# Kernel tuning notes

Measured on AMD Instinct MI355X. Metric: run time of the kernel, lower is better.

The kernel has to match this reference:

```python
import jax, jax.numpy as jnp
import numpy as np

B, N, IN_DIM, HID = 32, 1024, 128, 64


def setup_inputs() -> dict:
    key = jax.random.key(0)
    ks = jax.random.split(key, 12)
    s_in = 1.0 / np.sqrt(IN_DIM)
    s_h = 1.0 / np.sqrt(HID)
    return {
        "x": jax.random.normal(ks[0], (B, N, IN_DIM), dtype=jnp.float32),
        "A": jax.random.uniform(ks[1], (B, N, N), dtype=jnp.float32),
        # fc_hidden: input_dim -> hidden_dim
        "W_h": jax.random.uniform(ks[2], (IN_DIM, HID), jnp.float32, -s_in, s_in),
        "b_h": jax.random.uniform(ks[3], (HID,), jnp.float32, -s_in, s_in),
        # fc_1 inside Gated_Skip_Connection (input_dim != output_dim)
        "W_fc1": jax.random.uniform(ks[4], (IN_DIM, HID), jnp.float32, -s_in, s_in),
        "b_fc1": jax.random.uniform(ks[5], (HID,), jnp.float32, -s_in, s_in),
        # gated_X1, gated_X2: hidden -> hidden
        "W_g1": jax.random.uniform(ks[6], (HID, HID), jnp.float32, -s_h, s_h),
        "b_g1": jax.random.uniform(ks[7], (HID,), jnp.float32, -s_h, s_h),
        "W_g2": jax.random.uniform(ks[8], (HID, HID), jnp.float32, -s_h, s_h),
        "b_g2": jax.random.uniform(ks[9], (HID,), jnp.float32, -s_h, s_h),
    }


def reference(x, A, W_h, b_h, W_fc1, b_fc1, W_g1, b_g1, W_g2, b_g2):
    # x_new = bmm(A, fc_hidden(x))   [B, N, HID]
    x_new = jnp.einsum("bnm,bmh->bnh", A, x @ W_h + b_h)
    # gated skip connection (input_dim != output_dim -> project x first)
    x_proj = x @ W_fc1 + b_fc1
    gate = jax.nn.sigmoid((x_proj @ W_g1 + b_g1) + (x_new @ W_g2 + b_g2))
    out = x_new * gate + x_proj * (1.0 - gate)
    return out
```

## Files before the change

### kernel.cpp

```cpp
#include <hip/hip_runtime.h>
#include <hip/hip_bf16.h>

#define NB 32
#define NN 1024
#define IND 128
#define HD 64

typedef float f32x4 __attribute__((ext_vector_type(4)));
typedef short bf16x8 __attribute__((ext_vector_type(8)));
typedef unsigned short ushortx4 __attribute__((ext_vector_type(4)));

union FragU { unsigned short us[8]; unsigned int u32[4]; bf16x8 v; };

__device__ __forceinline__ unsigned short f2bf(float f) {
    union { float f; unsigned u; } x; x.f = f;
    unsigned r = x.u + 0x7FFFu + ((x.u >> 16) & 1u);
    return (unsigned short)(r >> 16);
}
__device__ __forceinline__ float bf2f(unsigned short h) {
    union { unsigned u; float f; } x; x.u = ((unsigned)h) << 16; return x.f;
}
__device__ __forceinline__ unsigned int cvtpk(float lo, float hi) {
    unsigned int r;
    asm("v_cvt_pk_bf16_f32 %0, %1, %2" : "=v"(r) : "v"(lo), "v"(hi));
    return r;
}

__device__ __forceinline__ void gl16(void* lds, const void* g) {
    __builtin_amdgcn_global_load_lds(
        (const __attribute__((address_space(1))) unsigned int*)g,
        (__attribute__((address_space(3))) unsigned int*)lds, 16, 0, 0);
}

__global__ void prep_k(const float* __restrict__ W_h, const float* __restrict__ W_fc1,
                       const float* __restrict__ W_g1, const float* __restrict__ W_g2,
                       const float* __restrict__ b_g1, const float* __restrict__ b_g2,
                       unsigned short* __restrict__ WcT_hi, unsigned short* __restrict__ WcT_lo,
                       unsigned short* __restrict__ Wg1T_hi, unsigned short* __restrict__ Wg1T_lo,
                       unsigned short* __restrict__ Wg2T_hi, unsigned short* __restrict__ Wg2T_lo,
                       float* __restrict__ biasP1) {
    int t = blockIdx.x * blockDim.x + threadIdx.x;
    if (t < 16384) {
        int o = t >> 7, k = t & 127;
        float v = (o < 64) ? W_h[k * 64 + o] : W_fc1[k * 64 + (o - 64)];
        unsigned short hi = f2bf(v);
        WcT_hi[t] = hi; WcT_lo[t] = f2bf(v - bf2f(hi));
    } else if (t < 20480) {
        int r = t - 16384; int o = r >> 6, k = r & 63;
        float v = W_g1[k * 64 + o];
        unsigned short hi = f2bf(v);
        Wg1T_hi[r] = hi; Wg1T_lo[r] = f2bf(v - bf2f(hi));
    } else if (t < 24576) {
        int r = t - 20480; int o = r >> 6, k = r & 63;
        float v = W_g2[k * 64 + o];
        unsigned short hi = f2bf(v);
        Wg2T_hi[r] = hi; Wg2T_lo[r] = f2bf(v - bf2f(hi));
    } else if (t < 24640) {
        int j = t - 24576;
        biasP1[j] = b_g1[j] + b_g2[j];
    }
}

__global__ __launch_bounds__(64) void k1(
        const float* __restrict__ x,
        const unsigned short* __restrict__ WcT_hi, const unsigned short* __restrict__ WcT_lo,
        const unsigned short* __restrict__ Wg1T_hi, const unsigned short* __restrict__ Wg1T_lo,
        const float* __restrict__ b_h, const float* __restrict__ b_fc1,
        const float* __restrict__ biasP1,
        unsigned short* __restrict__ hF, float* __restrict__ xproj,
        float* __restrict__ p1) {
    __shared__ unsigned short lds_hi[16 * 64];
    __shared__ unsigned short lds_lo[16 * 64];

    const int lane = threadIdx.x;
    const int lr = lane & 15, lg = lane >> 4;
    const int blk = blockIdx.x;
    const int b = blk >> 6;
    const int n0 = (blk & 63) * 16;

    const float* xp = x + (size_t)(b * NN + n0 + lr) * IND;

    f32x4 xa[4][2];
#pragma unroll
    for (int ks = 0; ks < 4; ks++) {
        const f32x4* ap = (const f32x4*)(xp + 32 * ks + 8 * lg);
        xa[ks][0] = ap[0]; xa[ks][1] = ap[1];
    }

    f32x4 acc[8];
#pragma unroll
    for (int f = 0; f < 8; f++) acc[f] = (f32x4){0.f, 0.f, 0.f, 0.f};

#pragma unroll
    for (int ks = 0; ks < 4; ks++) {
        FragU ah, al;
#pragma unroll
        for (int i = 0; i < 4; i++) {
            unsigned short h0 = f2bf(xa[ks][0][i]); ah.us[i] = h0;     al.us[i]     = f2bf(xa[ks][0][i] - bf2f(h0));
            unsigned short h1 = f2bf(xa[ks][1][i]); ah.us[4 + i] = h1; al.us[4 + i] = f2bf(xa[ks][1][i] - bf2f(h1));
        }
#pragma unroll
        for (int f = 0; f < 8; f++) {
            int off = (16 * f + lr) * 128 + 32 * ks + 8 * lg;
            bf16x8 wh = *(const bf16x8*)(WcT_hi + off);
            bf16x8 wl = *(const bf16x8*)(WcT_lo + off);
            acc[f] = __builtin_amdgcn_mfma_f32_16x16x32_bf16(ah.v, wh, acc[f], 0, 0, 0);
            acc[f] = __builtin_amdgcn_mfma_f32_16x16x32_bf16(ah.v, wl, acc[f], 0, 0, 0);
            acc[f] = __builtin_amdgcn_mfma_f32_16x16x32_bf16(al.v, wh, acc[f], 0, 0, 0);
        }
    }

    const int mb = n0 + 4 * lg;
    const int tile = mb >> 5;
    const int lanepart = lr + 16 * ((mb >> 3) & 3);
    const int j0 = mb & 7;

#pragma unroll
    for (int f = 0; f < 4; f++) {
        int c = 16 * f + lr;
        float bh = b_h[c];
        ushortx4 hv;
#pragma unroll
        for (int r = 0; r < 4; r++) hv[r] = f2bf(acc[f][r] + bh);
        *(ushortx4*)(hF + (size_t)b * 65536 + (size_t)(tile * 4 + f) * 512 + lanepart * 8 + j0) = hv;
    }

#pragma unroll
    for (int f = 4; f < 8; f++) {
        int c = 16 * (f - 4) + lr;
        float bp = b_fc1[c];
#pragma unroll
        for (int r = 0; r < 4; r++) {
            float v = acc[f][r] + bp;
            int n = mb + r;
            xproj[(size_t)(b * NN + n) * 64 + c] = v;
            int ln = 4 * lg + r;
            int idx = ln * 64 + (((c >> 3) ^ (ln & 7)) << 3) + (c & 7);
            unsigned short hi = f2bf(v);
            lds_hi[idx] = hi;
            lds_lo[idx] = f2bf(v - bf2f(hi));
        }
    }
    __syncthreads();

    f32x4 accP[4];
#pragma unroll
    for (int f = 0; f < 4; f++) accP[f] = (f32x4){0.f, 0.f, 0.f, 0.f};
#pragma unroll
    for (int ks = 0; ks < 2; ks++) {
        int c0 = 32 * ks + 8 * lg;
        int idx = lr * 64 + (((c0 >> 3) ^ (lr & 7)) << 3);
        bf16x8 a_hi = *(const bf16x8*)(lds_hi + idx);
        bf16x8 a_lo = *(const bf16x8*)(lds_lo + idx);
#pragma unroll
        for (int f = 0; f < 4; f++) {
            int off = (16 * f + lr) * 64 + c0;
            bf16x8 b_hi = *(const bf16x8*)(Wg1T_hi + off);
            bf16x8 b_lo = *(const bf16x8*)(Wg1T_lo + off);
            accP[f] = __builtin_amdgcn_mfma_f32_16x16x32_bf16(a_hi, b_hi, accP[f], 0, 0, 0);
            accP[f] = __builtin_amdgcn_mfma_f32_16x16x32_bf16(a_hi, b_lo, accP[f], 0, 0, 0);
            accP[f] = __builtin_amdgcn_mfma_f32_16x16x32_bf16(a_lo, b_hi, accP[f], 0, 0, 0);
        }
    }
#pragma unroll
    for (int f = 0; f < 4; f++) {
        int c = 16 * f + lr;
        float bb = biasP1[c];
#pragma unroll
        for (int r = 0; r < 4; r++) {
            int n = mb + r;
            p1[(size_t)(b * NN + n) * 64 + c] = accP[f][r] + bb;
        }
    }
}

__global__ __launch_bounds__(256, 4) void k2(
        const float* __restrict__ A, const unsigned short* __restrict__ hF,
        const unsigned short* __restrict__ Wg2T_hi, const unsigned short* __restrict__ Wg2T_lo,
        const float* __restrict__ p1, const float* __restrict__ xproj,
        float* __restrict__ out) {
    __shared__ char smem[36864];

    const int tid = threadIdx.x;
    const int w = tid >> 6, lane = tid & 63;
    const int lr = lane & 15, lg = lane >> 4;

    const int bid = blockIdx.x;
    const int wgid = (bid & 7) * 128 + (bid >> 3);
    const int b = wgid >> 5;
    const int blkst = wgid & 31;

    const float* aS[4];
#pragma unroll
    for (int i = 0; i < 4; i++) {
        int rl = w * 4 + i;
        aS[i] = A + (size_t)(b * NN + blkst * 32 + rl) * NN + ((lane ^ rl) << 2);
    }
    const unsigned short* hp = hF + (size_t)b * 65536 + w * 512 + lane * 8;

    bf16x8 hb[8];

#pragma unroll
    for (int i = 0; i < 4; i++)
        gl16(smem + (w * 4 + i) * 1024, aS[i]);
#pragma unroll
    for (int ks = 0; ks < 8; ks++)
        hb[ks] = *(const bf16x8*)(hp + (size_t)ks * 2048);
    __syncthreads();

#define COMPUTE(ks, Abase)                                                     \
    {                                                                          \
        int g0 = (ks) * 8 + lg * 2;                                            \
        f32x4 a0 = *(const f32x4*)((Abase) + ((g0 ^ lr) << 4));                \
        f32x4 a1 = *(const f32x4*)((Abase) + (((g0 + 1) ^ lr) << 4));          \
        FragU au;                                                              \
        au.u32[0] = cvtpk(a0[0], a0[1]); au.u32[1] = cvtpk(a0[2], a0[3]);      \
        au.u32[2] = cvtpk(a1[0], a1[1]); au.u32[3] = cvtpk(a1[2], a1[3]);      \
        acc = __builtin_amdgcn_mfma_f32_16x16x32_bf16(au.v, hb[ks], acc, 0, 0, 0); \
    }

#pragma unroll
    for (int s = 0; s < 2; s++) {
        f32x4 acc = (f32x4){0.f, 0.f, 0.f, 0.f};
        f32x4 pv, xv;

#pragma unroll
        for (int t = 0; t < 4; t++) {
            const char* Abase = smem + (t & 1) * 16384 + lr * 1024;
            const bool last = (s == 1) && (t == 3);
            if (!last) {
                const size_t soff = (t < 3) ? ((size_t)s * 16384 + (t + 1) * 256)
                                            : ((size_t)(s + 1) * 16384);
#pragma unroll
                for (int i = 0; i < 4; i++)
                    gl16(smem + ((t + 1) & 1) * 16384 + (w * 4 + i) * 1024,
                         aS[i] + soff);
            }
            const int tn = (t < 3) ? (t + 1) : 0;

            COMPUTE(0, Abase) COMPUTE(1, Abase) COMPUTE(2, Abase) COMPUTE(3, Abase)
            if (!last) {
#pragma unroll
                for (int ks = 0; ks < 4; ks++)
                    hb[ks] = *(const bf16x8*)(hp + (size_t)(tn * 8 + ks) * 2048);
            }
            COMPUTE(4, Abase) COMPUTE(5, Abase) COMPUTE(6, Abase) COMPUTE(7, Abase)
            if (!last) {
#pragma unroll
                for (int ks = 4; ks < 8; ks++)
                    hb[ks] = *(const bf16x8*)(hp + (size_t)(tn * 8 + ks) * 2048);
            }
            if (t == 3) {
                const int c = 16 * w + lr;
                const int nbase = (blkst * 2 + s) * 16 + 4 * lg;
                const float* pp = p1    + (size_t)(b * NN + nbase) * 64 + c;
                const float* xp = xproj + (size_t)(b * NN + nbase) * 64 + c;
#pragma unroll
                for (int r = 0; r < 4; r++) { pv[r] = pp[r * 64]; xv[r] = xp[r * 64]; }
            }
            __syncthreads();
        }

        unsigned short* th = (unsigned short*)(smem + 32768);
        unsigned short* tl = th + 1024;
        {
            int c = 16 * w + lr;
#pragma unroll
            for (int r = 0; r < 4; r++) {
                int row = 4 * lg + r;
                int idx = row * 64 + (((c >> 3) ^ (row & 7)) << 3) + (c & 7);
                float v = acc[r];
                unsigned short hi = f2bf(v);
                th[idx] = hi;
                tl[idx] = f2bf(v - bf2f(hi));
            }
        }
        __syncthreads();

        f32x4 accG = (f32x4){0.f, 0.f, 0.f, 0.f};
#pragma unroll
        for (int ksk = 0; ksk < 2; ksk++) {
            int c0k = 32 * ksk + 8 * lg;
            int idx = lr * 64 + (((c0k >> 3) ^ (lr & 7)) << 3);
            bf16x8 a_hi = *(const bf16x8*)(th + idx);
            bf16x8 a_lo = *(const bf16x8*)(tl + idx);
            int off = (16 * w + lr) * 64 + c0k;
            bf16x8 b_hi = *(const bf16x8*)(Wg2T_hi + off);
            bf16x8 b_lo = *(const bf16x8*)(Wg2T_lo + off);
            accG = __builtin_amdgcn_mfma_f32_16x16x32_bf16(a_hi, b_hi, accG, 0, 0, 0);
            accG = __builtin_amdgcn_mfma_f32_16x16x32_bf16(a_hi, b_lo, accG, 0, 0, 0);
            accG = __builtin_amdgcn_mfma_f32_16x16x32_bf16(a_lo, b_hi, accG, 0, 0, 0);
        }

        {
            int c = 16 * w + lr;
#pragma unroll
            for (int r = 0; r < 4; r++) {
                int n = (blkst * 2 + s) * 16 + 4 * lg + r;
                size_t g = (size_t)(b * NN + n) * 64 + c;
                float z = pv[r] + accG[r];
                float gate = 1.f / (1.f + __expf(-z));
                out[g] = acc[r] * gate + xv[r] * (1.f - gate);
            }
        }
        __syncthreads();
    }
#undef COMPUTE
}

extern "C" void kernel_launch(void* const* d_in, const int* in_sizes, int n_in,
                              void* d_out, int out_size, void* d_ws, size_t ws_size,
                              hipStream_t stream) {
    const float* x     = (const float*)d_in[0];
    const float* A     = (const float*)d_in[1];
    const float* W_h   = (const float*)d_in[2];
    const float* b_h   = (const float*)d_in[3];
    const float* W_fc1 = (const float*)d_in[4];
    const float* b_fc1 = (const float*)d_in[5];
    const float* W_g1  = (const float*)d_in[6];
    const float* b_g1  = (const float*)d_in[7];
    const float* W_g2  = (const float*)d_in[8];
    const float* b_g2  = (const float*)d_in[9];
    float* out = (float*)d_out;

    char* ws = (char*)d_ws;
    unsigned short* WcT_hi  = (unsigned short*)(ws);
    unsigned short* WcT_lo  = (unsigned short*)(ws + 32768);
    unsigned short* Wg1T_hi = (unsigned short*)(ws + 65536);
    unsigned short* Wg1T_lo = (unsigned short*)(ws + 73728);
    unsigned short* Wg2T_hi = (unsigned short*)(ws + 81920);
    unsigned short* Wg2T_lo = (unsigned short*)(ws + 90112);
    float*          bP1     = (float*)(ws + 98304);
    unsigned short* hF      = (unsigned short*)(ws + 131072);
    float*          xprj    = (float*)(ws + 131072 + 4194304);
    float*          p1      = (float*)(ws + 131072 + 4194304 + 8388608);

    prep_k<<<97, 256, 0, stream>>>(W_h, W_fc1, W_g1, W_g2, b_g1, b_g2,
                                   WcT_hi, WcT_lo, Wg1T_hi, Wg1T_lo, Wg2T_hi, Wg2T_lo, bP1);
    k1<<<2048, 64, 0, stream>>>(x, WcT_hi, WcT_lo, Wg1T_hi, Wg1T_lo, b_h, b_fc1, bP1,
                                hF, xprj, p1);
    k2<<<1024, 256, 0, stream>>>(A, hF, Wg2T_hi, Wg2T_lo, p1, xprj, out);
}
```

Measured before the change: 63.25 us.

## Move x_proj and gate-1 projection from k1 into k2 epilogue

k1 now only computes the hidden projection hF. k2 reloads x rows, computes x_proj with split-bf16 MFMAs, and folds the x_proj @ W_g1 term into the gate accumulator. This removes the fp32 xproj and p1 intermediates (about 8 MB each written and then read back). In exchange k2 does extra MFMA work and more LDS traffic, and loads x (16 MB) in its epilogue.

```diff
diff --git a/kernel.cpp b/kernel.cpp
--- a/kernel.cpp
+++ b/kernel.cpp
@@ -64,14 +64,8 @@
 __global__ __launch_bounds__(64) void k1(
         const float* __restrict__ x,
         const unsigned short* __restrict__ WcT_hi, const unsigned short* __restrict__ WcT_lo,
-        const unsigned short* __restrict__ Wg1T_hi, const unsigned short* __restrict__ Wg1T_lo,
-        const float* __restrict__ b_h, const float* __restrict__ b_fc1,
-        const float* __restrict__ biasP1,
-        unsigned short* __restrict__ hF, float* __restrict__ xproj,
-        float* __restrict__ p1) {
-    __shared__ unsigned short lds_hi[16 * 64];
-    __shared__ unsigned short lds_lo[16 * 64];
-
+        const float* __restrict__ b_h,
+        unsigned short* __restrict__ hF) {
     const int lane = threadIdx.x;
     const int lr = lane & 15, lg = lane >> 4;
     const int blk = blockIdx.x;
@@ -87,9 +81,9 @@
         xa[ks][0] = ap[0]; xa[ks][1] = ap[1];
     }
 
-    f32x4 acc[8];
-#pragma unroll
-    for (int f = 0; f < 8; f++) acc[f] = (f32x4){0.f, 0.f, 0.f, 0.f};
+    f32x4 acc[4];
+#pragma unroll
+    for (int f = 0; f < 4; f++) acc[f] = (f32x4){0.f, 0.f, 0.f, 0.f};
 
 #pragma unroll
     for (int ks = 0; ks < 4; ks++) {
@@ -100,7 +94,7 @@
             unsigned short h1 = f2bf(xa[ks][1][i]); ah.us[4 + i] = h1; al.us[4 + i] = f2bf(xa[ks][1][i] - bf2f(h1));
         }
 #pragma unroll
-        for (int f = 0; f < 8; f++) {
+        for (int f = 0; f < 4; f++) {
             int off = (16 * f + lr) * 128 + 32 * ks + 8 * lg;
             bf16x8 wh = *(const bf16x8*)(WcT_hi + off);
             bf16x8 wl = *(const bf16x8*)(WcT_lo + off);
@@ -124,62 +118,17 @@
         for (int r = 0; r < 4; r++) hv[r] = f2bf(acc[f][r] + bh);
         *(ushortx4*)(hF + (size_t)b * 65536 + (size_t)(tile * 4 + f) * 512 + lanepart * 8 + j0) = hv;
     }
-
-#pragma unroll
-    for (int f = 4; f < 8; f++) {
-        int c = 16 * (f - 4) + lr;
-        float bp = b_fc1[c];
-#pragma unroll
-        for (int r = 0; r < 4; r++) {
-            float v = acc[f][r] + bp;
-            int n = mb + r;
-            xproj[(size_t)(b * NN + n) * 64 + c] = v;
-            int ln = 4 * lg + r;
-            int idx = ln * 64 + (((c >> 3) ^ (ln & 7)) << 3) + (c & 7);
-            unsigned short hi = f2bf(v);
-            lds_hi[idx] = hi;
-            lds_lo[idx] = f2bf(v - bf2f(hi));
-        }
-    }
-    __syncthreads();
-
-    f32x4 accP[4];
-#pragma unroll
-    for (int f = 0; f < 4; f++) accP[f] = (f32x4){0.f, 0.f, 0.f, 0.f};
-#pragma unroll
-    for (int ks = 0; ks < 2; ks++) {
-        int c0 = 32 * ks + 8 * lg;
-        int idx = lr * 64 + (((c0 >> 3) ^ (lr & 7)) << 3);
-        bf16x8 a_hi = *(const bf16x8*)(lds_hi + idx);
-        bf16x8 a_lo = *(const bf16x8*)(lds_lo + idx);
-#pragma unroll
-        for (int f = 0; f < 4; f++) {
-            int off = (16 * f + lr) * 64 + c0;
-            bf16x8 b_hi = *(const bf16x8*)(Wg1T_hi + off);
-            bf16x8 b_lo = *(const bf16x8*)(Wg1T_lo + off);
-            accP[f] = __builtin_amdgcn_mfma_f32_16x16x32_bf16(a_hi, b_hi, accP[f], 0, 0, 0);
-            accP[f] = __builtin_amdgcn_mfma_f32_16x16x32_bf16(a_hi, b_lo, accP[f], 0, 0, 0);
-            accP[f] = __builtin_amdgcn_mfma_f32_16x16x32_bf16(a_lo, b_hi, accP[f], 0, 0, 0);
-        }
-    }
-#pragma unroll
-    for (int f = 0; f < 4; f++) {
-        int c = 16 * f + lr;
-        float bb = biasP1[c];
-#pragma unroll
-        for (int r = 0; r < 4; r++) {
-            int n = mb + r;
-            p1[(size_t)(b * NN + n) * 64 + c] = accP[f][r] + bb;
-        }
-    }
 }
 
 __global__ __launch_bounds__(256, 4) void k2(
         const float* __restrict__ A, const unsigned short* __restrict__ hF,
+        const unsigned short* __restrict__ WcT_hi, const unsigned short* __restrict__ WcT_lo,
+        const unsigned short* __restrict__ Wg1T_hi, const unsigned short* __restrict__ Wg1T_lo,
         const unsigned short* __restrict__ Wg2T_hi, const unsigned short* __restrict__ Wg2T_lo,
-        const float* __restrict__ p1, const float* __restrict__ xproj,
+        const float* __restrict__ biasP1, const float* __restrict__ b_fc1,
+        const float* __restrict__ x,
         float* __restrict__ out) {
-    __shared__ char smem[36864];
+    __shared__ char smem[32768];
 
     const int tid = threadIdx.x;
     const int w = tid >> 6, lane = tid & 63;
@@ -222,7 +171,7 @@
 #pragma unroll
     for (int s = 0; s < 2; s++) {
         f32x4 acc = (f32x4){0.f, 0.f, 0.f, 0.f};
-        f32x4 pv, xv;
+        f32x4 xfr[4][2];
 
 #pragma unroll
         for (int t = 0; t < 4; t++) {
@@ -251,29 +200,55 @@
                     hb[ks] = *(const bf16x8*)(hp + (size_t)(tn * 8 + ks) * 2048);
             }
             if (t == 3) {
-                const int c = 16 * w + lr;
-                const int nbase = (blkst * 2 + s) * 16 + 4 * lg;
-                const float* pp = p1    + (size_t)(b * NN + nbase) * 64 + c;
-                const float* xp = xproj + (size_t)(b * NN + nbase) * 64 + c;
-#pragma unroll
-                for (int r = 0; r < 4; r++) { pv[r] = pp[r * 64]; xv[r] = xp[r * 64]; }
+                const float* xp = x + (size_t)(b * NN + (blkst * 2 + s) * 16 + lr) * IND;
+#pragma unroll
+                for (int ks = 0; ks < 4; ks++) {
+                    xfr[ks][0] = *(const f32x4*)(xp + 32 * ks + 8 * lg);
+                    xfr[ks][1] = *(const f32x4*)(xp + 32 * ks + 8 * lg + 4);
+                }
             }
             __syncthreads();
         }
 
-        unsigned short* th = (unsigned short*)(smem + 32768);
+        f32x4 accX = (f32x4){0.f, 0.f, 0.f, 0.f};
+#pragma unroll
+        for (int ks = 0; ks < 4; ks++) {
+            FragU xh, xl;
+#pragma unroll
+            for (int i = 0; i < 4; i++) {
+                unsigned short h0 = f2bf(xfr[ks][0][i]); xh.us[i] = h0;     xl.us[i]     = f2bf(xfr[ks][0][i] - bf2f(h0));
+                unsigned short h1 = f2bf(xfr[ks][1][i]); xh.us[4 + i] = h1; xl.us[4 + i] = f2bf(xfr[ks][1][i] - bf2f(h1));
+            }
+            int off = (64 + 16 * w + lr) * 128 + 32 * ks + 8 * lg;
+            bf16x8 wh = *(const bf16x8*)(WcT_hi + off);
+            bf16x8 wl = *(const bf16x8*)(WcT_lo + off);
+            accX = __builtin_amdgcn_mfma_f32_16x16x32_bf16(xh.v, wh, accX, 0, 0, 0);
+            accX = __builtin_amdgcn_mfma_f32_16x16x32_bf16(xh.v, wl, accX, 0, 0, 0);
+            accX = __builtin_amdgcn_mfma_f32_16x16x32_bf16(xl.v, wh, accX, 0, 0, 0);
+        }
+        const int c = 16 * w + lr;
+        {
+            float bfc = b_fc1[c];
+#pragma unroll
+            for (int r = 0; r < 4; r++) accX[r] += bfc;
+        }
+
+        unsigned short* th = (unsigned short*)(smem + 16384);
         unsigned short* tl = th + 1024;
-        {
-            int c = 16 * w + lr;
-#pragma unroll
-            for (int r = 0; r < 4; r++) {
-                int row = 4 * lg + r;
-                int idx = row * 64 + (((c >> 3) ^ (row & 7)) << 3) + (c & 7);
-                float v = acc[r];
-                unsigned short hi = f2bf(v);
-                th[idx] = hi;
-                tl[idx] = f2bf(v - bf2f(hi));
-            }
+        unsigned short* uh = tl + 1024;
+        unsigned short* ul = uh + 1024;
+#pragma unroll
+        for (int r = 0; r < 4; r++) {
+            int row = 4 * lg + r;
+            int idx = row * 64 + (((c >> 3) ^ (row & 7)) << 3) + (c & 7);
+            float v = acc[r];
+            unsigned short hv = f2bf(v);
+            th[idx] = hv;
+            tl[idx] = f2bf(v - bf2f(hv));
+            float u = accX[r];
+            unsigned short hu = f2bf(u);
+            uh[idx] = hu;
+            ul[idx] = f2bf(u - bf2f(hu));
         }
         __syncthreads();
 
@@ -282,25 +257,32 @@
         for (int ksk = 0; ksk < 2; ksk++) {
             int c0k = 32 * ksk + 8 * lg;
             int idx = lr * 64 + (((c0k >> 3) ^ (lr & 7)) << 3);
-            bf16x8 a_hi = *(const bf16x8*)(th + idx);
-            bf16x8 a_lo = *(const bf16x8*)(tl + idx);
+            bf16x8 n_hi = *(const bf16x8*)(th + idx);
+            bf16x8 n_lo = *(const bf16x8*)(tl + idx);
+            bf16x8 p_hi = *(const bf16x8*)(uh + idx);
+            bf16x8 p_lo = *(const bf16x8*)(ul + idx);
             int off = (16 * w + lr) * 64 + c0k;
-            bf16x8 b_hi = *(const bf16x8*)(Wg2T_hi + off);
-            bf16x8 b_lo = *(const bf16x8*)(Wg2T_lo + off);
-            accG = __builtin_amdgcn_mfma_f32_16x16x32_bf16(a_hi, b_hi, accG, 0, 0, 0);
-            accG = __builtin_amdgcn_mfma_f32_16x16x32_bf16(a_hi, b_lo, accG, 0, 0, 0);
-            accG = __builtin_amdgcn_mfma_f32_16x16x32_bf16(a_lo, b_hi, accG, 0, 0, 0);
+            bf16x8 g2h = *(const bf16x8*)(Wg2T_hi + off);
+            bf16x8 g2l = *(const bf16x8*)(Wg2T_lo + off);
+            bf16x8 g1h = *(const bf16x8*)(Wg1T_hi + off);
+            bf16x8 g1l = *(const bf16x8*)(Wg1T_lo + off);
+            accG = __builtin_amdgcn_mfma_f32_16x16x32_bf16(n_hi, g2h, accG, 0, 0, 0);
+            accG = __builtin_amdgcn_mfma_f32_16x16x32_bf16(n_hi, g2l, accG, 0, 0, 0);
+            accG = __builtin_amdgcn_mfma_f32_16x16x32_bf16(n_lo, g2h, accG, 0, 0, 0);
+            accG = __builtin_amdgcn_mfma_f32_16x16x32_bf16(p_hi, g1h, accG, 0, 0, 0);
+            accG = __builtin_amdgcn_mfma_f32_16x16x32_bf16(p_hi, g1l, accG, 0, 0, 0);
+            accG = __builtin_amdgcn_mfma_f32_16x16x32_bf16(p_lo, g1h, accG, 0, 0, 0);
         }
 
         {
-            int c = 16 * w + lr;
+            float bb = biasP1[c];
 #pragma unroll
             for (int r = 0; r < 4; r++) {
                 int n = (blkst * 2 + s) * 16 + 4 * lg + r;
                 size_t g = (size_t)(b * NN + n) * 64 + c;
-                float z = pv[r] + accG[r];
+                float z = accG[r] + bb;
                 float gate = 1.f / (1.f + __expf(-z));
-                out[g] = acc[r] * gate + xv[r] * (1.f - gate);
+                out[g] = acc[r] * gate + accX[r] * (1.f - gate);
             }
         }
         __syncthreads();
@@ -332,12 +314,10 @@
     unsigned short* Wg2T_lo = (unsigned short*)(ws + 90112);
     float*          bP1     = (float*)(ws + 98304);
     unsigned short* hF      = (unsigned short*)(ws + 131072);
-    float*          xprj    = (float*)(ws + 131072 + 4194304);
-    float*          p1      = (float*)(ws + 131072 + 4194304 + 8388608);
 
     prep_k<<<97, 256, 0, stream>>>(W_h, W_fc1, W_g1, W_g2, b_g1, b_g2,
                                    WcT_hi, WcT_lo, Wg1T_hi, Wg1T_lo, Wg2T_hi, Wg2T_lo, bP1);
-    k1<<<2048, 64, 0, stream>>>(x, WcT_hi, WcT_lo, Wg1T_hi, Wg1T_lo, b_h, b_fc1, bP1,
-                                hF, xprj, p1);
-    k2<<<1024, 256, 0, stream>>>(A, hF, Wg2T_hi, Wg2T_lo, p1, xprj, out);
-}
+    k1<<<2048, 64, 0, stream>>>(x, WcT_hi, WcT_lo, b_h, hF);
+    k2<<<1024, 256, 0, stream>>>(A, hF, WcT_hi, WcT_lo, Wg1T_hi, Wg1T_lo,
+                                 Wg2T_hi, Wg2T_lo, bP1, b_fc1, x, out);
+}
```

Result: slower. 68.40 us (+8.1%).
